# Kernel tuning notes

Measured on AMD Instinct MI355X. Metric: run time of the kernel, lower is better.

Reference implementation:

```python
import jax, jax.numpy as jnp
import numpy as np

V, H, T, B, S = 50000, 256, 32, 64, 512


def setup_inputs() -> dict:
    key = jax.random.key(0)
    ks = jax.random.split(key, 16)
    sc = 0.05
    def n(k, shape):
        return jax.random.normal(k, shape, dtype=jnp.float32) * sc
    return {
        "seq": jax.random.randint(ks[0], (B, S), 0, V),
        "mask": jnp.ones((B, S), dtype=jnp.int32),
        "labels": jax.random.randint(ks[1], (B, S), 0, T),
        "embedding": n(ks[2], (V, H)),
        "Wih_f": n(ks[3], (4 * H, H)), "Whh_f": n(ks[4], (4 * H, H)),
        "bih_f": n(ks[5], (4 * H,)), "bhh_f": n(ks[6], (4 * H,)),
        "Wih_b": n(ks[7], (4 * H, H)), "Whh_b": n(ks[8], (4 * H, H)),
        "bih_b": n(ks[9], (4 * H,)), "bhh_b": n(ks[10], (4 * H,)),
        "fcW": n(ks[11], (T, 2 * H)), "fcb": n(ks[12], (T,)),
        "start_trans": n(ks[13], (T,)), "end_trans": n(ks[14], (T,)),
        "trans": n(ks[15], (T, T)),
    }


def _lstm_dir(x, Wih, Whh, bih, bhh, reverse):
    # x: [S,B,H]; torch LSTM gate order i,f,g,o
    Bz, Hh = x.shape[1], Whh.shape[1]
    def step(carry, xt):
        h, c = carry
        g = xt @ Wih.T + h @ Whh.T + bih + bhh  # [B,4H]
        i, f, gg, o = jnp.split(g, 4, axis=-1)
        c = jax.nn.sigmoid(f) * c + jax.nn.sigmoid(i) * jnp.tanh(gg)
        h = jax.nn.sigmoid(o) * jnp.tanh(c)
        return (h, c), h
    init = (jnp.zeros((Bz, Hh), x.dtype), jnp.zeros((Bz, Hh), x.dtype))
    _, hs = jax.lax.scan(step, init, x, reverse=reverse)
    return hs


def _crf_llh(em, tags, mask, start, end, trans):
    # em [S,B,T], tags [S,B] int, mask [S,B] bool -> scalar sum log-likelihood
    Sx, Bx, Tx = em.shape
    barange = jnp.arange(Bx)
    em_sc = jnp.take_along_axis(em, tags[:, :, None], axis=2)[..., 0]  # [S,B]
    m = mask.astype(em.dtype)
    num = start[tags[0]] + em_sc[0]
    tr_sc = trans[tags[:-1], tags[1:]]  # [S-1,B]
    num = num + jnp.sum((tr_sc + em_sc[1:]) * m[1:], axis=0)
    seq_ends = jnp.sum(mask.astype(jnp.int32), axis=0) - 1
    last_tags = tags[seq_ends, barange]
    num = num + end[last_tags]
    # forward algorithm (log-partition)
    def step(score, em_m):
        em_t, m_t = em_m
        nxt = jax.nn.logsumexp(score[:, :, None] + trans[None], axis=1) + em_t
        return jnp.where(m_t[:, None], nxt, score), None
    score0 = start[None] + em[0]
    score, _ = jax.lax.scan(step, score0, (em[1:], mask[1:]))
    den = jax.nn.logsumexp(score + end[None], axis=1)
    return jnp.sum(num - den)


def _viterbi(em, mask, start, end, trans):
    Sx, Bx, Tx = em.shape
    def step(score, em_m):
        em_t, m_t = em_m
        cand = score[:, :, None] + trans[None]  # [B,T_prev,T_cur]
        idx = jnp.argmax(cand, axis=1)
        nxt = jnp.max(cand, axis=1) + em_t
        idx = jnp.where(m_t[:, None], idx, jnp.arange(Tx)[None])
        return jnp.where(m_t[:, None], nxt, score), idx
    score0 = start[None] + em[0]
    score, hist = jax.lax.scan(step, score0, (em[1:], mask[1:]))  # hist [S-1,B,T]
    last = jnp.argmax(score + end[None], axis=1)  # [B]
    barange = jnp.arange(Bx)
    def back(tag, idx_t):
        prev = idx_t[barange, tag]
        return prev, prev
    _, prevs = jax.lax.scan(back, last, hist, reverse=True)  # prevs[k] = tag at time k
    return jnp.concatenate([prevs, last[None]], axis=0)  # [S,B]


def reference(seq, mask, labels, embedding, Wih_f, Whh_f, bih_f, bhh_f,
              Wih_b, Whh_b, bih_b, bhh_b, fcW, fcb,
              start_trans, end_trans, trans):
    x = seq.T  # [S,B] time-major as in original
    emb = embedding[x]  # [S,B,H]
    hf = _lstm_dir(emb, Wih_f, Whh_f, bih_f, bhh_f, False)
    hb = _lstm_dir(emb, Wih_b, Whh_b, bih_b, bhh_b, True)
    out = jnp.concatenate([hf, hb], axis=-1)  # [S,B,2H]
    logits = out @ fcW.T + fcb  # [S,B,T]; dropout is identity at eval
    m = mask.T.astype(bool)  # [S,B]
    loss = -_crf_llh(logits, labels.T, m, start_trans, end_trans, trans)
    preds = _viterbi(logits, m, start_trans, end_trans, trans)  # [S,B]
    return preds.T, loss
```

## Files before the change

kernel.cpp:

```cpp
#include <hip/hip_runtime.h>
#include <stdint.h>

#define SS 512
#define BB 64
#define HH 256
#define TT 32

typedef __attribute__((ext_vector_type(8))) short bf16x8;
typedef __attribute__((ext_vector_type(4))) short short4v;
typedef __attribute__((ext_vector_type(4))) float f32x4;

__device__ __forceinline__ unsigned short f2bf(float f){
  unsigned u = __float_as_uint(f);
  unsigned r = (u + 0x7FFFu + ((u >> 16) & 1u)) >> 16;
  return (unsigned short)r;
}
__device__ __forceinline__ float bf2f(unsigned short s){
  return __uint_as_float(((unsigned)s) << 16);
}
__device__ __forceinline__ float sigm(float x){ return 1.0f/(1.0f+__expf(-x)); }
__device__ __forceinline__ float ftanh(float x){
  float e = __expf(2.f*x);
  return 1.f - 2.f/(e + 1.f);
}
__device__ __forceinline__ unsigned cvt4fp8(float a0, float a1, float a2, float a3){
  int d = __builtin_amdgcn_cvt_pk_fp8_f32(a0, a1, 0, false);
  d = __builtin_amdgcn_cvt_pk_fp8_f32(a2, a3, d, true);
  return (unsigned)d;
}
__device__ __forceinline__ unsigned char cvt1fp8(float a){
  int d = __builtin_amdgcn_cvt_pk_fp8_f32(a, a, 0, false);
  return (unsigned char)(d & 0xFF);
}

__device__ __forceinline__ bf16x8 afrag(const unsigned short* A, int mt, int ktp, int nl, int kq){
  int m = mt*16 + nl;
  int sw = (m & 7) << 3;
  int kk = ktp*32 + kq*4;
  short4v lo = *(const short4v*)(A + (m << 8) + (kk ^ sw));
  short4v hi = *(const short4v*)(A + (m << 8) + ((kk + 16) ^ sw));
  bf16x8 r = {lo[0],lo[1],lo[2],lo[3],hi[0],hi[1],hi[2],hi[3]};
  return r;
}

__global__ __launch_bounds__(256,1) void k_xgemm(
    const int* __restrict__ seq, const float* __restrict__ emb,
    const float* __restrict__ Wih_f, const float* __restrict__ Wih_b,
    unsigned short* __restrict__ gx)
{
  __shared__ __align__(16) unsigned short A_l[128*256];
  __shared__ __align__(16) unsigned short B_l[64*256];

  const int tid = threadIdx.x;
  const int lane = tid & 63, w = tid >> 6;
  const int nl = lane & 15, kq = lane >> 4;
  const int pbase = blockIdx.x * 128;
  const int dir = blockIdx.y;
  const float* Wih = dir ? Wih_b : Wih_f;

#pragma unroll
  for (int i = 0; i < 16; ++i){
    int c = tid + i*256;
    int m = c >> 5, k8 = c & 31;
    int p = pbase + m, t = p >> 6, b = p & 63;
    int er = seq[b*SS + t];
    const float* s = emb + (size_t)er*HH + k8*8;
    float4 x0 = *(const float4*)s, x1 = *(const float4*)(s+4);
    union { unsigned short u[8]; uint4 v; } o;
    o.u[0]=f2bf(x0.x); o.u[1]=f2bf(x0.y); o.u[2]=f2bf(x0.z); o.u[3]=f2bf(x0.w);
    o.u[4]=f2bf(x1.x); o.u[5]=f2bf(x1.y); o.u[6]=f2bf(x1.z); o.u[7]=f2bf(x1.w);
    *(uint4*)&A_l[(m << 8) + ((k8*8) ^ ((m & 7) << 3))] = o.v;
  }

  for (int nb = 0; nb < 16; ++nb){
    __syncthreads();
#pragma unroll
    for (int i = 0; i < 8; ++i){
      int c = tid + i*256;
      int m = c >> 5, k8 = c & 31;
      const float* s = Wih + (size_t)(nb*64 + m)*HH + k8*8;
      float4 x0 = *(const float4*)s, x1 = *(const float4*)(s+4);
      union { unsigned short u[8]; uint4 v; } o;
      o.u[0]=f2bf(x0.x); o.u[1]=f2bf(x0.y); o.u[2]=f2bf(x0.z); o.u[3]=f2bf(x0.w);
      o.u[4]=f2bf(x1.x); o.u[5]=f2bf(x1.y); o.u[6]=f2bf(x1.z); o.u[7]=f2bf(x1.w);
      *(uint4*)&B_l[(m << 8) + ((k8*8) ^ ((m & 7) << 3))] = o.v;
    }
    __syncthreads();

    f32x4 acc[2][4];
#pragma unroll
    for (int mt = 0; mt < 2; ++mt)
#pragma unroll
      for (int nt = 0; nt < 4; ++nt) acc[mt][nt] = (f32x4){0.f,0.f,0.f,0.f};

#pragma unroll
    for (int kt = 0; kt < 8; ++kt){
      bf16x8 a0 = afrag(A_l, w*2+0, kt, nl, kq);
      bf16x8 a1 = afrag(A_l, w*2+1, kt, nl, kq);
#pragma unroll
      for (int nt = 0; nt < 4; ++nt){
        bf16x8 bv = afrag(B_l, nt, kt, nl, kq);
        acc[0][nt] = __builtin_amdgcn_mfma_f32_16x16x32_bf16(a0, bv, acc[0][nt], 0,0,0);
        acc[1][nt] = __builtin_amdgcn_mfma_f32_16x16x32_bf16(a1, bv, acc[1][nt], 0,0,0);
      }
    }

#pragma unroll
    for (int mt = 0; mt < 2; ++mt)
#pragma unroll
      for (int nt = 0; nt < 4; ++nt){
        int p0 = pbase + w*32 + mt*16 + kq*4;
        int t = p0 >> 6, b0 = p0 & 63;
        int col = nb*64 + nt*16 + nl;
        union { unsigned short u[4]; uint2 v; } o;
        o.u[0]=f2bf(acc[mt][nt][0]); o.u[1]=f2bf(acc[mt][nt][1]);
        o.u[2]=f2bf(acc[mt][nt][2]); o.u[3]=f2bf(acc[mt][nt][3]);
        *(uint2*)(gx + ((size_t)(dir*16 + (b0 >> 2))*SS + t)*4096 + col*4) = o.v;
      }
  }
}

#define WSC 64.0f
#define HSC 16.0f
#define ISC (1.0f/(WSC*HSC))

__global__ __launch_bounds__(512,1) void k_lstm(
    const unsigned short* __restrict__ gx,
    const float* __restrict__ Whh_f, const float* __restrict__ bih_f, const float* __restrict__ bhh_f,
    const float* __restrict__ Whh_b, const float* __restrict__ bih_b, const float* __restrict__ bhh_b,
    unsigned short* __restrict__ hf, unsigned short* __restrict__ hb)
{
  __shared__ __align__(16) unsigned char h8[2][16][272];
  __shared__ __align__(16) float xch[8][4][2][16][4];

  const int tid  = threadIdx.x;
  const int lane = tid & 63;
  const int w    = tid >> 6;
  const int nl   = lane & 15;
  const int kq   = lane >> 4;
  const int dir  = blockIdx.x >> 4;
  const int bg   = blockIdx.x & 15;

  const float* Whh = dir ? Whh_b : Whh_f;
  const float* bih = dir ? bih_b : bih_f;
  const float* bhh = dir ? bhh_b : bhh_f;
  unsigned short* hbuf = dir ? hb : hf;
  const unsigned short* gxd = gx + (size_t)(dir*16 + bg)*SS*4096;

  long wB[4][2][8];
#pragma unroll
  for (int g = 0; g < 4; ++g)
#pragma unroll
    for (int q = 0; q < 2; ++q)
#pragma unroll
      for (int kt = 0; kt < 8; ++kt){
        int ncol = g*256 + w*32 + q*16 + nl;
        const float* p = Whh + (size_t)ncol*HH + kt*32 + kq*4;
        float4 lo = *(const float4*)p;
        float4 hi = *(const float4*)(p + 16);
        union { unsigned d[2]; long l; } u;
        u.d[0] = cvt4fp8(lo.x*WSC, lo.y*WSC, lo.z*WSC, lo.w*WSC);
        u.d[1] = cvt4fp8(hi.x*WSC, hi.y*WSC, hi.z*WSC, hi.w*WSC);
        wB[g][q][kt] = u.l;
      }

  float bias_c[4][2];
#pragma unroll
  for (int g = 0; g < 4; ++g)
#pragma unroll
    for (int q = 0; q < 2; ++q){
      int col = g*256 + w*32 + q*16 + nl;
      bias_c[g][q] = bih[col] + bhh[col];
    }
  const int bp0 = w*32 + (nl >> 2)*8 + (nl & 3);
  const int bp1 = bp0 + 4;

  for (int i = tid; i < 2176; i += 512) ((unsigned*)h8)[i] = 0;
  __syncthreads();

  float c0 = 0.f, c1 = 0.f;

  unsigned short gxc[4][2], gxn[4][2];
  {
    const int t0 = dir ? (SS-1) : 0;
    const unsigned short* gp = gxd + (size_t)t0*4096;
#pragma unroll
    for (int g = 0; g < 4; ++g)
#pragma unroll
      for (int q = 0; q < 2; ++q)
        gxc[g][q] = gp[(g*256 + w*32 + q*16 + nl)*4 + kq];
  }

  for (int s = 0; s < SS; ++s){
    const int t = dir ? (SS-1-s) : s;

    {
      int sn = s + 1;
      int tn = (sn < SS) ? (dir ? (SS-1-sn) : sn) : t;
      const unsigned short* gp = gxd + (size_t)tn*4096;
#pragma unroll
      for (int g = 0; g < 4; ++g)
#pragma unroll
        for (int q = 0; q < 2; ++q)
          gxn[g][q] = gp[(g*256 + w*32 + q*16 + nl)*4 + kq];
    }

    const unsigned char* tp8 = &h8[s & 1][0][0];
    long af[8];
#pragma unroll
    for (int kt = 0; kt < 8; ++kt)
      af[kt] = *(const long*)(tp8 + nl*272 + kt*32 + kq*8);

    f32x4 acc[4][2];
#pragma unroll
    for (int g = 0; g < 4; ++g)
#pragma unroll
      for (int q = 0; q < 2; ++q) acc[g][q] = (f32x4){0.f,0.f,0.f,0.f};

#pragma unroll
    for (int kt = 0; kt < 8; ++kt)
#pragma unroll
      for (int g = 0; g < 4; ++g)
#pragma unroll
        for (int q = 0; q < 2; ++q)
          acc[g][q] = __builtin_amdgcn_mfma_f32_16x16x32_fp8_fp8(af[kt], wB[g][q][kt], acc[g][q], 0,0,0);

    if (kq == 0){
#pragma unroll
      for (int g = 0; g < 4; ++g)
#pragma unroll
        for (int q = 0; q < 2; ++q)
          *(f32x4*)&xch[w][g][q][nl][0] = acc[g][q];
    }
    asm volatile("s_waitcnt lgkmcnt(0)" ::: "memory");

    {
      const int wslot = dir ? t : (s + 1);
      unsigned short* hrow = hbuf + (size_t)(wslot*BB + bg*4 + kq)*HH + w*32 + nl;
      unsigned char* arow = &h8[(s + 1) & 1][kq][0];
#pragma unroll
      for (int q = 0; q < 2; ++q){
        float i_ = xch[w][0][q][nl][kq]*ISC + bf2f(gxc[0][q]) + bias_c[0][q];
        float f_ = xch[w][1][q][nl][kq]*ISC + bf2f(gxc[1][q]) + bias_c[1][q];
        float g_ = xch[w][2][q][nl][kq]*ISC + bf2f(gxc[2][q]) + bias_c[2][q];
        float o_ = xch[w][3][q][nl][kq]*ISC + bf2f(gxc[3][q]) + bias_c[3][q];
        float cold = q ? c1 : c0;
        float cnew = sigm(f_)*cold + sigm(i_)*ftanh(g_);
        if (q) c1 = cnew; else c0 = cnew;
        float h = sigm(o_)*ftanh(cnew);
        hrow[q*16] = f2bf(h);
        arow[q ? bp1 : bp0] = cvt1fp8(h*HSC);
      }
    }

#pragma unroll
    for (int g = 0; g < 4; ++g)
#pragma unroll
      for (int q = 0; q < 2; ++q) gxc[g][q] = gxn[g][q];

    asm volatile("s_waitcnt lgkmcnt(0)" ::: "memory");
    __builtin_amdgcn_s_barrier();
    asm volatile("" ::: "memory");
  }
}

__global__ __launch_bounds__(256,1) void k_fc(
    const unsigned short* __restrict__ hf, const unsigned short* __restrict__ hb,
    const float* __restrict__ fcW, const float* __restrict__ fcb,
    float* __restrict__ logits)
{
  __shared__ unsigned short Bs[32][516];
  __shared__ unsigned short Ah[4][32][260];
  __shared__ float fcb_s[32];
  const int tid = threadIdx.x;
  for (int i = tid; i < 32*512; i += 256){
    int tg = i >> 9, k = i & 511;
    Bs[tg][k] = f2bf(fcW[tg*512 + k]);
  }
  if (tid < 32) fcb_s[tid] = fcb[tid];
  __syncthreads();

  const int lane = tid & 63, w = tid >> 6;
  const int nl = lane & 15, kq = lane >> 4;
  const int pbase = blockIdx.x * 128;

  f32x4 acc[2][2];
#pragma unroll
  for (int mt = 0; mt < 2; ++mt)
#pragma unroll
    for (int nt = 0; nt < 2; ++nt) acc[mt][nt] = (f32x4){0.f,0.f,0.f,0.f};

  for (int half = 0; half < 2; ++half){
    for (int rr = 0; rr < 32; ++rr){
      int p = pbase + w*32 + rr;
      int t = p >> 6, b = p & 63;
      const unsigned short* src = half ? (hb + (size_t)(t*BB + b)*HH)
                                       : (hf + (size_t)((t+1)*BB + b)*HH);
      *(uint2*)&Ah[w][rr][lane*4] = *(const uint2*)(src + lane*4);
    }
#pragma unroll
    for (int kt = 0; kt < 8; ++kt){
      int kl = kt*32 + kq*4;
      bf16x8 a[2];
#pragma unroll
      for (int mt = 0; mt < 2; ++mt){
        const unsigned short* ar = &Ah[w][mt*16 + nl][kl];
        short4v lo = *(const short4v*)ar;
        short4v hi = *(const short4v*)(ar + 16);
        bf16x8 f = {lo[0],lo[1],lo[2],lo[3],hi[0],hi[1],hi[2],hi[3]};
        a[mt] = f;
      }
#pragma unroll
      for (int nt = 0; nt < 2; ++nt){
        const unsigned short* br = &Bs[nt*16 + nl][half*256 + kl];
        short4v lo = *(const short4v*)br;
        short4v hi = *(const short4v*)(br + 16);
        bf16x8 bv = {lo[0],lo[1],lo[2],lo[3],hi[0],hi[1],hi[2],hi[3]};
        acc[0][nt] = __builtin_amdgcn_mfma_f32_16x16x32_bf16(a[0], bv, acc[0][nt], 0,0,0);
        acc[1][nt] = __builtin_amdgcn_mfma_f32_16x16x32_bf16(a[1], bv, acc[1][nt], 0,0,0);
      }
    }
  }
#pragma unroll
  for (int mt = 0; mt < 2; ++mt)
#pragma unroll
    for (int nt = 0; nt < 2; ++nt)
#pragma unroll
      for (int r = 0; r < 4; ++r){
        int p = pbase + w*32 + mt*16 + kq*4 + r;
        int tg = nt*16 + nl;
        logits[(size_t)p*TT + tg] = acc[mt][nt][r] + fcb_s[tg];
      }
}

__global__ void k_crf(const float* __restrict__ logits, const int* __restrict__ mask,
                      const int* __restrict__ labels,
                      const float* __restrict__ start, const float* __restrict__ endt,
                      const float* __restrict__ trans,
                      float* __restrict__ den, float* __restrict__ num,
                      float* __restrict__ preds)
{
  __shared__ float tr[1024];
  __shared__ unsigned char vh_l[4][SS-1][32];
  const int tid = threadIdx.x;
  const int role = blockIdx.x >> 4;
  const int bq   = blockIdx.x & 15;
  if (role != 2){
    for (int i = tid; i < 1024; i += 256) tr[i] = trans[i];
    __syncthreads();
  }
  const int lane = tid & 63, w = tid >> 6;
  const int b = bq*4 + w;
  const int grp = lane >> 5, tp = lane & 31;

  if (role == 0){
    float score = start[tp] + logits[(size_t)b*TT + tp];
    float em_c = logits[(size_t)(BB + b)*TT + tp];
    int   mk_c = mask[b*SS + 1];
    for (int s = 1; s < SS; ++s){
      int sn = (s + 1 < SS) ? s + 1 : s;
      float em_n = logits[(size_t)(sn*BB + b)*TT + tp];
      int   mk_n = mask[b*SS + sn];
      float m = -1e30f;
#pragma unroll
      for (int jj = 0; jj < 16; ++jj){
        int j = grp*16 + jj;
        float v = __shfl(score, j) + tr[j*32 + tp];
        m = fmaxf(m, v);
      }
      m = fmaxf(m, __shfl_xor(m, 32));
      float ssum = 0.f;
#pragma unroll
      for (int jj = 0; jj < 16; ++jj){
        int j = grp*16 + jj;
        float v = __shfl(score, j) + tr[j*32 + tp];
        ssum += __expf(v - m);
      }
      ssum += __shfl_xor(ssum, 32);
      float ns = m + __logf(ssum) + em_c;
      score = mk_c ? ns : score;
      em_c = em_n; mk_c = mk_n;
    }
    float v = score + endt[tp];
    float mm = v;
    for (int d = 1; d < 32; d <<= 1) mm = fmaxf(mm, __shfl_xor(mm, d));
    float se = __expf(v - mm);
    for (int d = 1; d < 32; d <<= 1) se += __shfl_xor(se, d);
    if (lane == 0) den[b] = mm + __logf(se);
  } else if (role == 1){
    float score = start[tp] + logits[(size_t)b*TT + tp];
    float em_c = logits[(size_t)(BB + b)*TT + tp];
    int   mk_c = mask[b*SS + 1];
    for (int s = 1; s < SS; ++s){
      int sn = (s + 1 < SS) ? s + 1 : s;
      float em_n = logits[(size_t)(sn*BB + b)*TT + tp];
      int   mk_n = mask[b*SS + sn];
      float m = -1e30f; int am = 0;
#pragma unroll
      for (int jj = 0; jj < 16; ++jj){
        int j = grp*16 + jj;
        float v = __shfl(score, j) + tr[j*32 + tp];
        if (v > m){ m = v; am = j; }
      }
      float om = __shfl_xor(m, 32); int oam = __shfl_xor(am, 32);
      if (om > m || (om == m && oam < am)){ m = om; am = oam; }
      float ns = m + em_c;
      int idx = mk_c ? am : tp;
      if (grp == 0) vh_l[w][s-1][tp] = (unsigned char)idx;
      score = mk_c ? ns : score;
      em_c = em_n; mk_c = mk_n;
    }
    float v = score + endt[tp]; int a = tp;
    for (int d = 1; d < 32; d <<= 1){
      float ov = __shfl_xor(v, d); int oa = __shfl_xor(a, d);
      if (ov > v || (ov == v && oa < a)){ v = ov; a = oa; }
    }
    int tag = __shfl(a, 0);
    if (lane == 0) preds[(size_t)b*SS + SS - 1] = (float)tag;
    for (int s = SS - 1; s >= 1; --s){
      int rv = vh_l[w][s-1][tp];
      int pv = __shfl(rv, tag);
      if (lane == 0) preds[(size_t)b*SS + s - 1] = (float)pv;
      tag = pv;
    }
  } else {
    float acc = 0.f; int mcnt = 0;
    for (int s = lane; s < SS; s += 64){
      int mk = mask[b*SS + s];
      mcnt += mk;
      if (s >= 1){
        int tg = labels[b*SS + s], tpp = labels[b*SS + s - 1];
        float v = trans[tpp*32 + tg] + logits[(size_t)(s*BB + b)*TT + tg];
        acc += mk ? v : 0.f;
      }
    }
    for (int d = 1; d < 64; d <<= 1){ acc += __shfl_xor(acc, d); mcnt += __shfl_xor(mcnt, d); }
    if (lane == 0){
      int t0 = labels[b*SS];
      int tl = labels[b*SS + (mcnt - 1)];
      num[b] = start[t0] + logits[(size_t)b*TT + t0] + acc + endt[tl];
    }
  }
}

__global__ void k_loss(const float* __restrict__ num, const float* __restrict__ den,
                       float* __restrict__ out)
{
  int l = threadIdx.x;
  float v = num[l] - den[l];
  for (int d = 1; d < 64; d <<= 1) v += __shfl_xor(v, d);
  if (l == 0) out[BB*SS] = -v;
}

extern "C" void kernel_launch(void* const* d_in, const int* in_sizes, int n_in,
                              void* d_out, int out_size, void* d_ws, size_t ws_size,
                              hipStream_t stream)
{
  const int*   seq       = (const int*)  d_in[0];
  const int*   mask      = (const int*)  d_in[1];
  const int*   labels    = (const int*)  d_in[2];
  const float* embedding = (const float*)d_in[3];
  const float* Wih_f     = (const float*)d_in[4];
  const float* Whh_f     = (const float*)d_in[5];
  const float* bih_f     = (const float*)d_in[6];
  const float* bhh_f     = (const float*)d_in[7];
  const float* Wih_b     = (const float*)d_in[8];
  const float* Whh_b     = (const float*)d_in[9];
  const float* bih_b     = (const float*)d_in[10];
  const float* bhh_b     = (const float*)d_in[11];
  const float* fcW       = (const float*)d_in[12];
  const float* fcb       = (const float*)d_in[13];
  const float* start_t   = (const float*)d_in[14];
  const float* end_t     = (const float*)d_in[15];
  const float* trans     = (const float*)d_in[16];

  char* ws = (char*)d_ws;
  size_t off = 0;
  unsigned short* gxb = (unsigned short*)(ws + off); off += (size_t)2*SS*1024*64*2;
  unsigned short* hf  = (unsigned short*)(ws + off); off += (size_t)(SS+1)*BB*HH*2;
  unsigned short* hb  = (unsigned short*)(ws + off); off += (size_t)(SS+1)*BB*HH*2;
  float*          lgt = (float*)(ws + off);          off += (size_t)SS*BB*TT*4;
  float*          den = (float*)(ws + off);          off += 256;
  float*          num = (float*)(ws + off);          off += 256;

  k_xgemm<<<dim3(256,2), 256, 0, stream>>>(seq, embedding, Wih_f, Wih_b, gxb);
  k_lstm<<<32, 512, 0, stream>>>(gxb, Whh_f, bih_f, bhh_f, Whh_b, bih_b, bhh_b, hf, hb);
  k_fc<<<256, 256, 0, stream>>>(hf, hb, fcW, fcb, lgt);
  k_crf<<<48, 256, 0, stream>>>(lgt, mask, labels, start_t, end_t, trans, den, num, (float*)d_out);
  k_loss<<<1, 64, 0, stream>>>(num, den, (float*)d_out);
}
```

Before: 1.530 ms.

## Process two batch groups per LSTM block to overlap MFMA with gate math

Halves the LSTM grid from 32 to 16 blocks, so each block steps two independent batch groups (A and B) through the recurrence. Group B's MFMA work can then overlap group A's elementwise gate computation, with s_setprio raising priority around the MFMA loops. The LSTM biases are folded into the input-projection GEMM epilogue, and h outputs are written as packed pairs: bf16 via v_cvt_pk_bf16_f32 and two fp8 values per store. Explicit memsets zero the initial h slots. The trade-off is fewer CUs in use and more serial work per block, which pays off only if the overlap hides enough of the per-step latency.

```diff
diff --git a/kernel.cpp b/kernel.cpp
--- a/kernel.cpp
+++ b/kernel.cpp
@@ -28,9 +28,9 @@
   d = __builtin_amdgcn_cvt_pk_fp8_f32(a2, a3, d, true);
   return (unsigned)d;
 }
-__device__ __forceinline__ unsigned char cvt1fp8(float a){
-  int d = __builtin_amdgcn_cvt_pk_fp8_f32(a, a, 0, false);
-  return (unsigned char)(d & 0xFF);
+__device__ __forceinline__ unsigned short cvt2fp8(float a0, float a1){
+  int d = __builtin_amdgcn_cvt_pk_fp8_f32(a0, a1, 0, false);
+  return (unsigned short)(d & 0xFFFF);
 }
 
 __device__ __forceinline__ bf16x8 afrag(const unsigned short* A, int mt, int ktp, int nl, int kq){
@@ -46,6 +46,8 @@
 __global__ __launch_bounds__(256,1) void k_xgemm(
     const int* __restrict__ seq, const float* __restrict__ emb,
     const float* __restrict__ Wih_f, const float* __restrict__ Wih_b,
+    const float* __restrict__ bih_f, const float* __restrict__ bhh_f,
+    const float* __restrict__ bih_b, const float* __restrict__ bhh_b,
     unsigned short* __restrict__ gx)
 {
   __shared__ __align__(16) unsigned short A_l[128*256];
@@ -56,7 +58,9 @@
   const int nl = lane & 15, kq = lane >> 4;
   const int pbase = blockIdx.x * 128;
   const int dir = blockIdx.y;
-  const float* Wih = dir ? Wih_b : Wih_f;
+  const float* Wih  = dir ? Wih_b : Wih_f;
+  const float* bihd = dir ? bih_b : bih_f;
+  const float* bhhd = dir ? bhh_b : bhh_f;
 
 #pragma unroll
   for (int i = 0; i < 16; ++i){
@@ -112,9 +116,10 @@
         int p0 = pbase + w*32 + mt*16 + kq*4;
         int t = p0 >> 6, b0 = p0 & 63;
         int col = nb*64 + nt*16 + nl;
+        float bs = bihd[col] + bhhd[col];
         union { unsigned short u[4]; uint2 v; } o;
-        o.u[0]=f2bf(acc[mt][nt][0]); o.u[1]=f2bf(acc[mt][nt][1]);
-        o.u[2]=f2bf(acc[mt][nt][2]); o.u[3]=f2bf(acc[mt][nt][3]);
+        o.u[0]=f2bf(acc[mt][nt][0] + bs); o.u[1]=f2bf(acc[mt][nt][1] + bs);
+        o.u[2]=f2bf(acc[mt][nt][2] + bs); o.u[3]=f2bf(acc[mt][nt][3] + bs);
         *(uint2*)(gx + ((size_t)(dir*16 + (b0 >> 2))*SS + t)*4096 + col*4) = o.v;
       }
   }
@@ -126,26 +131,26 @@
 
 __global__ __launch_bounds__(512,1) void k_lstm(
     const unsigned short* __restrict__ gx,
-    const float* __restrict__ Whh_f, const float* __restrict__ bih_f, const float* __restrict__ bhh_f,
-    const float* __restrict__ Whh_b, const float* __restrict__ bih_b, const float* __restrict__ bhh_b,
+    const float* __restrict__ Whh_f, const float* __restrict__ Whh_b,
     unsigned short* __restrict__ hf, unsigned short* __restrict__ hb)
 {
-  __shared__ __align__(16) unsigned char h8[2][16][272];
-  __shared__ __align__(16) float xch[8][4][2][16][4];
+  __shared__ __align__(16) unsigned char h8[2][2][16][272];
+  __shared__ __align__(16) float xchA[8][4][2][16][4];
+  __shared__ __align__(16) float xchB[8][4][2][16][4];
 
   const int tid  = threadIdx.x;
   const int lane = tid & 63;
   const int w    = tid >> 6;
   const int nl   = lane & 15;
   const int kq   = lane >> 4;
-  const int dir  = blockIdx.x >> 4;
-  const int bg   = blockIdx.x & 15;
+  const int dir  = blockIdx.x >> 3;
+  const int bp   = blockIdx.x & 7;
+  const int bgA  = bp*2, bgB = bp*2 + 1;
 
   const float* Whh = dir ? Whh_b : Whh_f;
-  const float* bih = dir ? bih_b : bih_f;
-  const float* bhh = dir ? bhh_b : bhh_f;
   unsigned short* hbuf = dir ? hb : hf;
-  const unsigned short* gxd = gx + (size_t)(dir*16 + bg)*SS*4096;
+  const unsigned short* gpA0 = gx + (size_t)(dir*16 + bgA)*SS*4096;
+  const unsigned short* gpB0 = gx + (size_t)(dir*16 + bgB)*SS*4096;
 
   long wB[4][2][8];
 #pragma unroll
@@ -164,31 +169,27 @@
         wB[g][q][kt] = u.l;
       }
 
-  float bias_c[4][2];
-#pragma unroll
-  for (int g = 0; g < 4; ++g)
-#pragma unroll
-    for (int q = 0; q < 2; ++q){
-      int col = g*256 + w*32 + q*16 + nl;
-      bias_c[g][q] = bih[col] + bhh[col];
-    }
-  const int bp0 = w*32 + (nl >> 2)*8 + (nl & 3);
-  const int bp1 = bp0 + 4;
-
-  for (int i = tid; i < 2176; i += 512) ((unsigned*)h8)[i] = 0;
+  const int c0  = w*32 + 2*nl;
+  const int q0  = nl >> 3;
+  const int nx0 = (2*nl) & 15, nx1 = (2*nl + 1) & 15;
+  const int hb8 = ((c0 & 15) >> 2)*8 + ((c0 & 16) ? 4 : 0) + (c0 & 3);
+  const int hbyte = w*32 + hb8;
+
+  for (int i = tid; i < 4352; i += 512) ((unsigned*)h8)[i] = 0;
   __syncthreads();
 
-  float c0 = 0.f, c1 = 0.f;
-
-  unsigned short gxc[4][2], gxn[4][2];
+  float cA[2] = {0.f,0.f}, cB[2] = {0.f,0.f};
+
+  unsigned short gxcA[4][2], gxcB[4][2], gxnA[4][2], gxnB[4][2];
   {
     const int t0 = dir ? (SS-1) : 0;
-    const unsigned short* gp = gxd + (size_t)t0*4096;
 #pragma unroll
     for (int g = 0; g < 4; ++g)
 #pragma unroll
-      for (int q = 0; q < 2; ++q)
-        gxc[g][q] = gp[(g*256 + w*32 + q*16 + nl)*4 + kq];
+      for (int j = 0; j < 2; ++j){
+        gxcA[g][j] = gpA0[((size_t)t0*4096) + (g*256 + c0 + j)*4 + kq];
+        gxcB[g][j] = gpB0[((size_t)t0*4096) + (g*256 + c0 + j)*4 + kq];
+      }
   }
 
   for (int s = 0; s < SS; ++s){
@@ -197,66 +198,130 @@
     {
       int sn = s + 1;
       int tn = (sn < SS) ? (dir ? (SS-1-sn) : sn) : t;
-      const unsigned short* gp = gxd + (size_t)tn*4096;
 #pragma unroll
       for (int g = 0; g < 4; ++g)
 #pragma unroll
+        for (int j = 0; j < 2; ++j){
+          gxnA[g][j] = gpA0[((size_t)tn*4096) + (g*256 + c0 + j)*4 + kq];
+          gxnB[g][j] = gpB0[((size_t)tn*4096) + (g*256 + c0 + j)*4 + kq];
+        }
+    }
+
+    const unsigned char* tA = &h8[0][s & 1][0][0];
+    const unsigned char* tB = &h8[1][s & 1][0][0];
+    long afA[8], afB[8];
+#pragma unroll
+    for (int kt = 0; kt < 8; ++kt){
+      afA[kt] = *(const long*)(tA + nl*272 + kt*32 + kq*8);
+      afB[kt] = *(const long*)(tB + nl*272 + kt*32 + kq*8);
+    }
+
+    f32x4 acc[4][2];
+#pragma unroll
+    for (int g = 0; g < 4; ++g)
+#pragma unroll
+      for (int q = 0; q < 2; ++q) acc[g][q] = (f32x4){0.f,0.f,0.f,0.f};
+
+    __builtin_amdgcn_s_setprio(1);
+#pragma unroll
+    for (int kt = 0; kt < 8; ++kt)
+#pragma unroll
+      for (int g = 0; g < 4; ++g)
+#pragma unroll
         for (int q = 0; q < 2; ++q)
-          gxn[g][q] = gp[(g*256 + w*32 + q*16 + nl)*4 + kq];
-    }
-
-    const unsigned char* tp8 = &h8[s & 1][0][0];
-    long af[8];
+          acc[g][q] = __builtin_amdgcn_mfma_f32_16x16x32_fp8_fp8(afA[kt], wB[g][q][kt], acc[g][q], 0,0,0);
+    __builtin_amdgcn_s_setprio(0);
+
+    if (kq == 0){
+#pragma unroll
+      for (int g = 0; g < 4; ++g)
+#pragma unroll
+        for (int q = 0; q < 2; ++q)
+          *(f32x4*)&xchA[w][g][q][nl][0] = acc[g][q];
+    }
+
+#pragma unroll
+    for (int g = 0; g < 4; ++g)
+#pragma unroll
+      for (int q = 0; q < 2; ++q) acc[g][q] = (f32x4){0.f,0.f,0.f,0.f};
+    __builtin_amdgcn_s_setprio(1);
 #pragma unroll
     for (int kt = 0; kt < 8; ++kt)
-      af[kt] = *(const long*)(tp8 + nl*272 + kt*32 + kq*8);
-
-    f32x4 acc[4][2];
-#pragma unroll
-    for (int g = 0; g < 4; ++g)
-#pragma unroll
-      for (int q = 0; q < 2; ++q) acc[g][q] = (f32x4){0.f,0.f,0.f,0.f};
-
-#pragma unroll
-    for (int kt = 0; kt < 8; ++kt)
 #pragma unroll
       for (int g = 0; g < 4; ++g)
 #pragma unroll
         for (int q = 0; q < 2; ++q)
-          acc[g][q] = __builtin_amdgcn_mfma_f32_16x16x32_fp8_fp8(af[kt], wB[g][q][kt], acc[g][q], 0,0,0);
-
-    if (kq == 0){
-#pragma unroll
-      for (int g = 0; g < 4; ++g)
-#pragma unroll
-        for (int q = 0; q < 2; ++q)
-          *(f32x4*)&xch[w][g][q][nl][0] = acc[g][q];
-    }
+          acc[g][q] = __builtin_amdgcn_mfma_f32_16x16x32_fp8_fp8(afB[kt], wB[g][q][kt], acc[g][q], 0,0,0);
+    __builtin_amdgcn_s_setprio(0);
+
     asm volatile("s_waitcnt lgkmcnt(0)" ::: "memory");
 
     {
       const int wslot = dir ? t : (s + 1);
-      unsigned short* hrow = hbuf + (size_t)(wslot*BB + bg*4 + kq)*HH + w*32 + nl;
-      unsigned char* arow = &h8[(s + 1) & 1][kq][0];
-#pragma unroll
-      for (int q = 0; q < 2; ++q){
-        float i_ = xch[w][0][q][nl][kq]*ISC + bf2f(gxc[0][q]) + bias_c[0][q];
-        float f_ = xch[w][1][q][nl][kq]*ISC + bf2f(gxc[1][q]) + bias_c[1][q];
-        float g_ = xch[w][2][q][nl][kq]*ISC + bf2f(gxc[2][q]) + bias_c[2][q];
-        float o_ = xch[w][3][q][nl][kq]*ISC + bf2f(gxc[3][q]) + bias_c[3][q];
-        float cold = q ? c1 : c0;
-        float cnew = sigm(f_)*cold + sigm(i_)*ftanh(g_);
-        if (q) c1 = cnew; else c0 = cnew;
-        float h = sigm(o_)*ftanh(cnew);
-        hrow[q*16] = f2bf(h);
-        arow[q ? bp1 : bp0] = cvt1fp8(h*HSC);
-      }
+      float h0, h1;
+      {
+        float i_ = xchA[w][0][q0][nx0][kq]*ISC + bf2f(gxcA[0][0]);
+        float f_ = xchA[w][1][q0][nx0][kq]*ISC + bf2f(gxcA[1][0]);
+        float g_ = xchA[w][2][q0][nx0][kq]*ISC + bf2f(gxcA[2][0]);
+        float o_ = xchA[w][3][q0][nx0][kq]*ISC + bf2f(gxcA[3][0]);
+        float cn = sigm(f_)*cA[0] + sigm(i_)*ftanh(g_);
+        cA[0] = cn; h0 = sigm(o_)*ftanh(cn);
+      }
+      {
+        float i_ = xchA[w][0][q0][nx1][kq]*ISC + bf2f(gxcA[0][1]);
+        float f_ = xchA[w][1][q0][nx1][kq]*ISC + bf2f(gxcA[1][1]);
+        float g_ = xchA[w][2][q0][nx1][kq]*ISC + bf2f(gxcA[2][1]);
+        float o_ = xchA[w][3][q0][nx1][kq]*ISC + bf2f(gxcA[3][1]);
+        float cn = sigm(f_)*cA[1] + sigm(i_)*ftanh(g_);
+        cA[1] = cn; h1 = sigm(o_)*ftanh(cn);
+      }
+      unsigned hv;
+      asm volatile("v_cvt_pk_bf16_f32 %0, %1, %2" : "=v"(hv) : "v"(h0), "v"(h1));
+      *(unsigned*)(hbuf + (size_t)(wslot*BB + bgA*4 + kq)*HH + c0) = hv;
+      *(unsigned short*)&h8[0][(s + 1) & 1][kq][hbyte] = cvt2fp8(h0*HSC, h1*HSC);
+    }
+
+    if (kq == 0){
+#pragma unroll
+      for (int g = 0; g < 4; ++g)
+#pragma unroll
+        for (int q = 0; q < 2; ++q)
+          *(f32x4*)&xchB[w][g][q][nl][0] = acc[g][q];
+    }
+    asm volatile("s_waitcnt lgkmcnt(0)" ::: "memory");
+
+    {
+      const int wslot = dir ? t : (s + 1);
+      float h0, h1;
+      {
+        float i_ = xchB[w][0][q0][nx0][kq]*ISC + bf2f(gxcB[0][0]);
+        float f_ = xchB[w][1][q0][nx0][kq]*ISC + bf2f(gxcB[1][0]);
+        float g_ = xchB[w][2][q0][nx0][kq]*ISC + bf2f(gxcB[2][0]);
+        float o_ = xchB[w][3][q0][nx0][kq]*ISC + bf2f(gxcB[3][0]);
+        float cn = sigm(f_)*cB[0] + sigm(i_)*ftanh(g_);
+        cB[0] = cn; h0 = sigm(o_)*ftanh(cn);
+      }
+      {
+        float i_ = xchB[w][0][q0][nx1][kq]*ISC + bf2f(gxcB[0][1]);
+        float f_ = xchB[w][1][q0][nx1][kq]*ISC + bf2f(gxcB[1][1]);
+        float g_ = xchB[w][2][q0][nx1][kq]*ISC + bf2f(gxcB[2][1]);
+        float o_ = xchB[w][3][q0][nx1][kq]*ISC + bf2f(gxcB[3][1]);
+        float cn = sigm(f_)*cB[1] + sigm(i_)*ftanh(g_);
+        cB[1] = cn; h1 = sigm(o_)*ftanh(cn);
+      }
+      unsigned hv;
+      asm volatile("v_cvt_pk_bf16_f32 %0, %1, %2" : "=v"(hv) : "v"(h0), "v"(h1));
+      *(unsigned*)(hbuf + (size_t)(wslot*BB + bgB*4 + kq)*HH + c0) = hv;
+      *(unsigned short*)&h8[1][(s + 1) & 1][kq][hbyte] = cvt2fp8(h0*HSC, h1*HSC);
     }
 
 #pragma unroll
     for (int g = 0; g < 4; ++g)
 #pragma unroll
-      for (int q = 0; q < 2; ++q) gxc[g][q] = gxn[g][q];
+      for (int j = 0; j < 2; ++j){
+        gxcA[g][j] = gxnA[g][j];
+        gxcB[g][j] = gxnB[g][j];
+      }
 
     asm volatile("s_waitcnt lgkmcnt(0)" ::: "memory");
     __builtin_amdgcn_s_barrier();
@@ -483,8 +548,12 @@
   float*          den = (float*)(ws + off);          off += 256;
   float*          num = (float*)(ws + off);          off += 256;
 
-  k_xgemm<<<dim3(256,2), 256, 0, stream>>>(seq, embedding, Wih_f, Wih_b, gxb);
-  k_lstm<<<32, 512, 0, stream>>>(gxb, Whh_f, bih_f, bhh_f, Whh_b, bih_b, bhh_b, hf, hb);
+  hipMemsetAsync(hf, 0, (size_t)BB*HH*2, stream);
+  hipMemsetAsync(hb + (size_t)SS*BB*HH, 0, (size_t)BB*HH*2, stream);
+
+  k_xgemm<<<dim3(256,2), 256, 0, stream>>>(seq, embedding, Wih_f, Wih_b,
+                                           bih_f, bhh_f, bih_b, bhh_b, gxb);
+  k_lstm<<<16, 512, 0, stream>>>(gxb, Whh_f, Whh_b, hf, hb);
   k_fc<<<256, 256, 0, stream>>>(hf, hb, fcW, fcb, lgt);
   k_crf<<<48, 256, 0, stream>>>(lgt, mask, labels, start_t, end_t, trans, den, num, (float*)d_out);
   k_loss<<<1, 64, 0, stream>>>(num, den, (float*)d_out);
```

After: 2.692 ms. 75.9% more time.

## Double LSTM block to 16 waves and fold biases into input GEMM

Applied to the files above, without the earlier changes.

The recurrent LSTM kernel now runs 1024 threads (16 waves) per block, each wave owning 16 hidden columns instead of 32. This halves the per-step MFMA chain and gate math per wave on the serial critical path. The bias sum (bih+bhh) is moved into the input-projection GEMM epilogue, so it is no longer added per step inside the recurrence. The cost is that more waves must synchronise at every time-step barrier, and the bias is now rounded to bf16 together with the gate preactivation.

```diff
diff --git a/kernel.cpp b/kernel.cpp
--- a/kernel.cpp
+++ b/kernel.cpp
@@ -46,6 +46,8 @@
 __global__ __launch_bounds__(256,1) void k_xgemm(
     const int* __restrict__ seq, const float* __restrict__ emb,
     const float* __restrict__ Wih_f, const float* __restrict__ Wih_b,
+    const float* __restrict__ bih_f, const float* __restrict__ bhh_f,
+    const float* __restrict__ bih_b, const float* __restrict__ bhh_b,
     unsigned short* __restrict__ gx)
 {
   __shared__ __align__(16) unsigned short A_l[128*256];
@@ -56,7 +58,9 @@
   const int nl = lane & 15, kq = lane >> 4;
   const int pbase = blockIdx.x * 128;
   const int dir = blockIdx.y;
-  const float* Wih = dir ? Wih_b : Wih_f;
+  const float* Wih  = dir ? Wih_b : Wih_f;
+  const float* bihd = dir ? bih_b : bih_f;
+  const float* bhhd = dir ? bhh_b : bhh_f;
 
 #pragma unroll
   for (int i = 0; i < 16; ++i){
@@ -112,9 +116,10 @@
         int p0 = pbase + w*32 + mt*16 + kq*4;
         int t = p0 >> 6, b0 = p0 & 63;
         int col = nb*64 + nt*16 + nl;
+        float bs = bihd[col] + bhhd[col];
         union { unsigned short u[4]; uint2 v; } o;
-        o.u[0]=f2bf(acc[mt][nt][0]); o.u[1]=f2bf(acc[mt][nt][1]);
-        o.u[2]=f2bf(acc[mt][nt][2]); o.u[3]=f2bf(acc[mt][nt][3]);
+        o.u[0]=f2bf(acc[mt][nt][0] + bs); o.u[1]=f2bf(acc[mt][nt][1] + bs);
+        o.u[2]=f2bf(acc[mt][nt][2] + bs); o.u[3]=f2bf(acc[mt][nt][3] + bs);
         *(uint2*)(gx + ((size_t)(dir*16 + (b0 >> 2))*SS + t)*4096 + col*4) = o.v;
       }
   }
@@ -124,14 +129,13 @@
 #define HSC 16.0f
 #define ISC (1.0f/(WSC*HSC))
 
-__global__ __launch_bounds__(512,1) void k_lstm(
+__global__ __launch_bounds__(1024,1) void k_lstm(
     const unsigned short* __restrict__ gx,
-    const float* __restrict__ Whh_f, const float* __restrict__ bih_f, const float* __restrict__ bhh_f,
-    const float* __restrict__ Whh_b, const float* __restrict__ bih_b, const float* __restrict__ bhh_b,
+    const float* __restrict__ Whh_f, const float* __restrict__ Whh_b,
     unsigned short* __restrict__ hf, unsigned short* __restrict__ hb)
 {
   __shared__ __align__(16) unsigned char h8[2][16][272];
-  __shared__ __align__(16) float xch[8][4][2][16][4];
+  __shared__ __align__(16) float xch[16][4][16][4];
 
   const int tid  = threadIdx.x;
   const int lane = tid & 63;
@@ -142,53 +146,39 @@
   const int bg   = blockIdx.x & 15;
 
   const float* Whh = dir ? Whh_b : Whh_f;
-  const float* bih = dir ? bih_b : bih_f;
-  const float* bhh = dir ? bhh_b : bhh_f;
   unsigned short* hbuf = dir ? hb : hf;
   const unsigned short* gxd = gx + (size_t)(dir*16 + bg)*SS*4096;
 
-  long wB[4][2][8];
+  long wB[4][8];
 #pragma unroll
   for (int g = 0; g < 4; ++g)
 #pragma unroll
-    for (int q = 0; q < 2; ++q)
-#pragma unroll
-      for (int kt = 0; kt < 8; ++kt){
-        int ncol = g*256 + w*32 + q*16 + nl;
-        const float* p = Whh + (size_t)ncol*HH + kt*32 + kq*4;
-        float4 lo = *(const float4*)p;
-        float4 hi = *(const float4*)(p + 16);
-        union { unsigned d[2]; long l; } u;
-        u.d[0] = cvt4fp8(lo.x*WSC, lo.y*WSC, lo.z*WSC, lo.w*WSC);
-        u.d[1] = cvt4fp8(hi.x*WSC, hi.y*WSC, hi.z*WSC, hi.w*WSC);
-        wB[g][q][kt] = u.l;
-      }
-
-  float bias_c[4][2];
-#pragma unroll
-  for (int g = 0; g < 4; ++g)
-#pragma unroll
-    for (int q = 0; q < 2; ++q){
-      int col = g*256 + w*32 + q*16 + nl;
-      bias_c[g][q] = bih[col] + bhh[col];
-    }
-  const int bp0 = w*32 + (nl >> 2)*8 + (nl & 3);
-  const int bp1 = bp0 + 4;
-
-  for (int i = tid; i < 2176; i += 512) ((unsigned*)h8)[i] = 0;
+    for (int kt = 0; kt < 8; ++kt){
+      int ncol = g*256 + w*16 + nl;
+      const float* p = Whh + (size_t)ncol*HH + kt*32 + kq*4;
+      float4 lo = *(const float4*)p;
+      float4 hi = *(const float4*)(p + 16);
+      union { unsigned d[2]; long l; } u;
+      u.d[0] = cvt4fp8(lo.x*WSC, lo.y*WSC, lo.z*WSC, lo.w*WSC);
+      u.d[1] = cvt4fp8(hi.x*WSC, hi.y*WSC, hi.z*WSC, hi.w*WSC);
+      wB[g][kt] = u.l;
+    }
+
+  const int cc = w*16 + nl;
+  const int hbyte = (cc >> 5)*32 + ((cc & 15) >> 2)*8 + ((cc & 16) ? 4 : 0) + (cc & 3);
+
+  for (int i = tid; i < 2176; i += 1024) ((unsigned*)h8)[i] = 0;
   __syncthreads();
 
-  float c0 = 0.f, c1 = 0.f;
-
-  unsigned short gxc[4][2], gxn[4][2];
+  float c0 = 0.f;
+
+  unsigned short gxc[4], gxn[4];
   {
     const int t0 = dir ? (SS-1) : 0;
     const unsigned short* gp = gxd + (size_t)t0*4096;
 #pragma unroll
     for (int g = 0; g < 4; ++g)
-#pragma unroll
-      for (int q = 0; q < 2; ++q)
-        gxc[g][q] = gp[(g*256 + w*32 + q*16 + nl)*4 + kq];
+      gxc[g] = gp[(g*256 + cc)*4 + kq];
   }
 
   for (int s = 0; s < SS; ++s){
@@ -200,9 +190,7 @@
       const unsigned short* gp = gxd + (size_t)tn*4096;
 #pragma unroll
       for (int g = 0; g < 4; ++g)
-#pragma unroll
-        for (int q = 0; q < 2; ++q)
-          gxn[g][q] = gp[(g*256 + w*32 + q*16 + nl)*4 + kq];
+        gxn[g] = gp[(g*256 + cc)*4 + kq];
     }
 
     const unsigned char* tp8 = &h8[s & 1][0][0];
@@ -211,52 +199,38 @@
     for (int kt = 0; kt < 8; ++kt)
       af[kt] = *(const long*)(tp8 + nl*272 + kt*32 + kq*8);
 
-    f32x4 acc[4][2];
-#pragma unroll
-    for (int g = 0; g < 4; ++g)
-#pragma unroll
-      for (int q = 0; q < 2; ++q) acc[g][q] = (f32x4){0.f,0.f,0.f,0.f};
+    f32x4 acc[4];
+#pragma unroll
+    for (int g = 0; g < 4; ++g) acc[g] = (f32x4){0.f,0.f,0.f,0.f};
 
 #pragma unroll
     for (int kt = 0; kt < 8; ++kt)
 #pragma unroll
       for (int g = 0; g < 4; ++g)
-#pragma unroll
-        for (int q = 0; q < 2; ++q)
-          acc[g][q] = __builtin_amdgcn_mfma_f32_16x16x32_fp8_fp8(af[kt], wB[g][q][kt], acc[g][q], 0,0,0);
+        acc[g] = __builtin_amdgcn_mfma_f32_16x16x32_fp8_fp8(af[kt], wB[g][kt], acc[g], 0,0,0);
 
     if (kq == 0){
 #pragma unroll
       for (int g = 0; g < 4; ++g)
-#pragma unroll
-        for (int q = 0; q < 2; ++q)
-          *(f32x4*)&xch[w][g][q][nl][0] = acc[g][q];
+        *(f32x4*)&xch[w][g][nl][0] = acc[g];
     }
     asm volatile("s_waitcnt lgkmcnt(0)" ::: "memory");
 
     {
       const int wslot = dir ? t : (s + 1);
-      unsigned short* hrow = hbuf + (size_t)(wslot*BB + bg*4 + kq)*HH + w*32 + nl;
-      unsigned char* arow = &h8[(s + 1) & 1][kq][0];
-#pragma unroll
-      for (int q = 0; q < 2; ++q){
-        float i_ = xch[w][0][q][nl][kq]*ISC + bf2f(gxc[0][q]) + bias_c[0][q];
-        float f_ = xch[w][1][q][nl][kq]*ISC + bf2f(gxc[1][q]) + bias_c[1][q];
-        float g_ = xch[w][2][q][nl][kq]*ISC + bf2f(gxc[2][q]) + bias_c[2][q];
-        float o_ = xch[w][3][q][nl][kq]*ISC + bf2f(gxc[3][q]) + bias_c[3][q];
-        float cold = q ? c1 : c0;
-        float cnew = sigm(f_)*cold + sigm(i_)*ftanh(g_);
-        if (q) c1 = cnew; else c0 = cnew;
-        float h = sigm(o_)*ftanh(cnew);
-        hrow[q*16] = f2bf(h);
-        arow[q ? bp1 : bp0] = cvt1fp8(h*HSC);
-      }
-    }
-
-#pragma unroll
-    for (int g = 0; g < 4; ++g)
-#pragma unroll
-      for (int q = 0; q < 2; ++q) gxc[g][q] = gxn[g][q];
+      float i_ = xch[w][0][nl][kq]*ISC + bf2f(gxc[0]);
+      float f_ = xch[w][1][nl][kq]*ISC + bf2f(gxc[1]);
+      float g_ = xch[w][2][nl][kq]*ISC + bf2f(gxc[2]);
+      float o_ = xch[w][3][nl][kq]*ISC + bf2f(gxc[3]);
+      float cn = sigm(f_)*c0 + sigm(i_)*ftanh(g_);
+      c0 = cn;
+      float h = sigm(o_)*ftanh(cn);
+      hbuf[(size_t)(wslot*BB + bg*4 + kq)*HH + cc] = f2bf(h);
+      h8[(s + 1) & 1][kq][hbyte] = cvt1fp8(h*HSC);
+    }
+
+#pragma unroll
+    for (int g = 0; g < 4; ++g) gxc[g] = gxn[g];
 
     asm volatile("s_waitcnt lgkmcnt(0)" ::: "memory");
     __builtin_amdgcn_s_barrier();
@@ -483,8 +457,9 @@
   float*          den = (float*)(ws + off);          off += 256;
   float*          num = (float*)(ws + off);          off += 256;
 
-  k_xgemm<<<dim3(256,2), 256, 0, stream>>>(seq, embedding, Wih_f, Wih_b, gxb);
-  k_lstm<<<32, 512, 0, stream>>>(gxb, Whh_f, bih_f, bhh_f, Whh_b, bih_b, bhh_b, hf, hb);
+  k_xgemm<<<dim3(256,2), 256, 0, stream>>>(seq, embedding, Wih_f, Wih_b,
+                                           bih_f, bhh_f, bih_b, bhh_b, gxb);
+  k_lstm<<<32, 1024, 0, stream>>>(gxb, Whh_f, Whh_b, hf, hb);
   k_fc<<<256, 256, 0, stream>>>(hf, hb, fcW, fcb, lgt);
   k_crf<<<48, 256, 0, stream>>>(lgt, mask, labels, start_t, end_t, trans, den, num, (float*)d_out);
   k_loss<<<1, 64, 0, stream>>>(num, den, (float*)d_out);
```

Result: faster. 1.449 ms, median of 2 (-5.3%).
